# Optimization experiments

Measured on AMD Instinct MI355X. Metric: run time of the kernel, lower is better.

## Reference

```python
import jax, jax.numpy as jnp
import numpy as np

TEMPERATURE = 8.0  # sqrt(d_k)=sqrt(64)
NEG = -1000000000.0

def setup_inputs() -> dict:
    key = jax.random.key(0)
    kq, kk, kv, km = jax.random.split(key, 4)
    BH, S, D = 64, 1024, 64
    q = jax.random.normal(kq, (BH, S, D), dtype=jnp.float32)
    k = jax.random.normal(kk, (BH, S, D), dtype=jnp.float32)
    v = jax.random.normal(kv, (BH, S, D), dtype=jnp.float32)
    mask = jax.random.randint(km, (BH, 1, S), 0, 2).astype(jnp.int32)
    return {"q": q, "k": k, "v": v, "mask": mask}

def reference(q, k, v, mask):
    # attn scores: [BH, S, S]
    attn = jnp.einsum('bqd,bkd->bqk', q / TEMPERATURE, k)
    attn = jnp.where(mask == 0, NEG, attn)
    attn = jax.nn.softmax(attn, axis=-1)
    output = jnp.einsum('bqk,bkd->bqd', attn, v)
    return (output, attn)
```

## Files before the change

kernel.cpp:

```cpp
#include <hip/hip_runtime.h>
#include <hip/hip_bf16.h>
#include <stdint.h>

typedef unsigned short u16;
typedef u16 u16x8 __attribute__((ext_vector_type(8)));
typedef u16x8 __attribute__((may_alias)) u16x8a;
typedef float f32x4 __attribute__((ext_vector_type(4)));
typedef f32x4 __attribute__((may_alias)) f32x4a;
typedef __bf16 bf16x8 __attribute__((ext_vector_type(8)));
typedef float f32x16 __attribute__((ext_vector_type(16)));

#define S_LEN 1024
#define D_DIM 64
#define BHN   64

__device__ __forceinline__ u16 f2bf(float f) {
  unsigned u = __builtin_bit_cast(unsigned, f);
  return (u16)((u + 0x7fffu + ((u >> 16) & 1u)) >> 16);
}
__device__ __forceinline__ float bf2f(u16 b) {
  return __builtin_bit_cast(float, (unsigned)b << 16);
}
__device__ __forceinline__ bf16x8 cvt8(const float* p) {
  f32x4 a = *reinterpret_cast<const f32x4a*>(p);
  f32x4 b = *reinterpret_cast<const f32x4a*>(p + 4);
  u16x8 r;
#pragma unroll
  for (int j = 0; j < 4; ++j) { r[j] = f2bf(a[j]); r[4 + j] = f2bf(b[j]); }
  return __builtin_bit_cast(bf16x8, r);
}
__device__ __forceinline__ bf16x8 ldbf(const u16* p) {
  return __builtin_bit_cast(bf16x8, *reinterpret_cast<const u16x8a*>(p));
}

#define SMEM_BYTES 35456
#define RS_OFF     34816
#define INV_OFF    (34816 + 512)

__global__ __launch_bounds__(256, 3) void attn_kernel(
    const float* __restrict__ Q, const float* __restrict__ K, const int* __restrict__ Mk,
    const float* __restrict__ V, float* __restrict__ outO, float* __restrict__ outA) {
  __shared__ __align__(16) char smem[SMEM_BYTES];
  const int tid = threadIdx.x;
  const int wave = tid >> 6, lane = tid & 63;
  const int l31 = lane & 31, half = lane >> 5;

  const int id = blockIdx.x;
  const int bh = (id & 7) * 8 + ((id >> 3) & 7);
  const int q0 = (id >> 6) << 5;

  u16* tbase = (u16*)smem;
  float* rs_lds = (float*)(smem + RS_OFF);
  float* inv_lds = (float*)(smem + INV_OFF);

  const float* qb = Q + (((size_t)bh << 10) + q0 + l31) * D_DIM + half * 8;
  bf16x8 qa[4];
#pragma unroll
  for (int ks = 0; ks < 4; ++ks) qa[ks] = cvt8(qb + ks * 16);

  const int colbase = wave * 256;
  const float* kb0 = K + ((size_t)bh << 10) * D_DIM + half * 8;
  const int* mrow = Mk + ((size_t)bh << 10) + colbase + l31;

  bf16x8 pfrag[16];
  float rs[16];
#pragma unroll
  for (int r = 0; r < 16; ++r) rs[r] = 0.0f;

#pragma unroll
  for (int t = 0; t < 8; ++t) {
    u16* tile = tbase + (((t & 1) << 2) + wave) * (32 * 40);
    const int col0 = colbase + t * 32;
    const float* kb = kb0 + (size_t)(col0 + l31) * D_DIM;
    f32x16 acc = 0.0f;
#pragma unroll
    for (int ks = 0; ks < 4; ++ks) {
      bf16x8 kf = cvt8(kb + ks * 16);
      acc = __builtin_amdgcn_mfma_f32_32x32x16_bf16(qa[ks], kf, acc, 0, 0, 0);
    }
    const float mf = (mrow[t * 32] == 0) ? 0.0f : 1.0f;
#pragma unroll
    for (int r = 0; r < 16; ++r) {
      float p = exp2f(acc[r] * 0.18033688f) * mf;
      u16 pb16 = f2bf(p);
      rs[r] += bf2f(pb16);
      const int row = (r & 3) + ((r >> 2) << 3) + (half << 2);
      tile[row * 40 + l31] = pb16;
    }
    __syncthreads();
    pfrag[2 * t]     = ldbf(tile + l31 * 40 + half * 8);
    pfrag[2 * t + 1] = ldbf(tile + l31 * 40 + 16 + half * 8);
  }

#pragma unroll
  for (int r = 0; r < 16; ++r) {
    float s = rs[r];
#pragma unroll
    for (int m = 1; m < 32; m <<= 1) s += __shfl_xor(s, m, 64);
    rs[r] = s;
  }
  if (l31 == 0) {
#pragma unroll
    for (int r = 0; r < 16; ++r) {
      const int row = (r & 3) + ((r >> 2) << 3) + (half << 2);
      rs_lds[wave * 32 + row] = rs[r];
    }
  }
  __syncthreads();
  if (tid < 32) {
    float s = rs_lds[tid] + rs_lds[32 + tid] + rs_lds[64 + tid] + rs_lds[96 + tid];
    inv_lds[tid] = 1.0f / s;
  }
  __syncthreads();

  f32x16 oacc0 = 0.0f, oacc1 = 0.0f;
  const float* vb = V + (((size_t)bh << 10) + colbase + half * 8) * D_DIM + l31;
#pragma unroll
  for (int kk = 0; kk < 16; ++kk) {
    u16x8 b0u, b1u;
#pragma unroll
    for (int j = 0; j < 8; ++j) {
      b0u[j] = f2bf(vb[(kk * 16 + j) * D_DIM]);
      b1u[j] = f2bf(vb[(kk * 16 + j) * D_DIM + 32]);
    }
    bf16x8 b0 = __builtin_bit_cast(bf16x8, b0u);
    bf16x8 b1 = __builtin_bit_cast(bf16x8, b1u);
    oacc0 = __builtin_amdgcn_mfma_f32_32x32x16_bf16(pfrag[kk], b0, oacc0, 0, 0, 0);
    oacc1 = __builtin_amdgcn_mfma_f32_32x32x16_bf16(pfrag[kk], b1, oacc1, 0, 0, 0);
  }

  const float myinv = inv_lds[l31];
  float* ab = outA + ((size_t)bh << 20) + ((size_t)(q0 + l31) << 10) + colbase + half * 8;
#pragma unroll
  for (int t = 0; t < 8; ++t) {
#pragma unroll
    for (int f = 0; f < 2; ++f) {
      bf16x8 pf = pfrag[2 * t + f];
      f32x4 lo, hi;
#pragma unroll
      for (int j = 0; j < 4; ++j) {
        lo[j] = (float)pf[j] * myinv;
        hi[j] = (float)pf[4 + j] * myinv;
      }
      *reinterpret_cast<f32x4a*>(ab + t * 32 + f * 16) = lo;
      *reinterpret_cast<f32x4a*>(ab + t * 32 + f * 16 + 4) = hi;
    }
  }

  float* ored = (float*)smem;
#pragma unroll
  for (int r = 0; r < 16; ++r) {
    const int row = (r & 3) + ((r >> 2) << 3) + (half << 2);
    ored[(wave * 32 + row) * 68 + l31] = oacc0[r];
    ored[(wave * 32 + row) * 68 + 32 + l31] = oacc1[r];
  }
  __syncthreads();
  const int orow = tid >> 3;
  const int oc = (tid & 7) * 8;
  const float iv = inv_lds[orow];
  f32x4 o0, o1;
#pragma unroll
  for (int j = 0; j < 8; ++j) {
    float o = ored[orow * 68 + oc + j] + ored[(32 + orow) * 68 + oc + j] +
              ored[(64 + orow) * 68 + oc + j] + ored[(96 + orow) * 68 + oc + j];
    float v = o * iv;
    if (j < 4) o0[j] = v; else o1[j - 4] = v;
  }
  float* ob = outO + (((size_t)bh << 10) + q0 + orow) * D_DIM + oc;
  *reinterpret_cast<f32x4a*>(ob) = o0;
  *reinterpret_cast<f32x4a*>(ob + 4) = o1;
}

extern "C" void kernel_launch(void* const* d_in, const int* in_sizes, int n_in,
                              void* d_out, int out_size, void* d_ws, size_t ws_size,
                              hipStream_t stream) {
  (void)in_sizes; (void)n_in; (void)out_size; (void)d_ws; (void)ws_size;
  const float* Q = (const float*)d_in[0];
  const float* K = (const float*)d_in[1];
  const float* V = (const float*)d_in[2];
  const int*   M = (const int*)d_in[3];
  float* outO = (float*)d_out;
  float* outA = outO + (size_t)BHN * S_LEN * D_DIM;

  attn_kernel<<<dim3(BHN * (S_LEN / 32)), dim3(256), 0, stream>>>(Q, K, M, V, outO, outA);
}
```

Before: 428.6 us.

## Shrink LDS via atomic output reduction, drop per-tile barriers, interleave attn stores

Replaces the four-wave output reduction buffer with a single shared accumulator updated by LDS float atomics. This shrinks shared memory so four blocks per CU can be requested instead of three. The per-tile __syncthreads is replaced by a wave-local lgkmcnt wait, which is valid because each wave writes and reads only its own tile. The block-to-(bh, q0) mapping is changed so that consecutive blocks on the same XCD share K/V, and attention-probability stores are interleaved into the PV MFMA loop. Native __bf16 conversions replace the manual rounding helpers. The LDS atomics add serialization, and the accumulator must be zeroed up front.

```diff
diff --git a/kernel.cpp b/kernel.cpp
--- a/kernel.cpp
+++ b/kernel.cpp
@@ -1,5 +1,4 @@
 #include <hip/hip_runtime.h>
-#include <hip/hip_bf16.h>
 #include <stdint.h>
 
 typedef unsigned short u16;
@@ -14,30 +13,24 @@
 #define D_DIM 64
 #define BHN   64
 
-__device__ __forceinline__ u16 f2bf(float f) {
-  unsigned u = __builtin_bit_cast(unsigned, f);
-  return (u16)((u + 0x7fffu + ((u >> 16) & 1u)) >> 16);
-}
-__device__ __forceinline__ float bf2f(u16 b) {
-  return __builtin_bit_cast(float, (unsigned)b << 16);
-}
 __device__ __forceinline__ bf16x8 cvt8(const float* p) {
   f32x4 a = *reinterpret_cast<const f32x4a*>(p);
   f32x4 b = *reinterpret_cast<const f32x4a*>(p + 4);
-  u16x8 r;
+  bf16x8 r;
 #pragma unroll
-  for (int j = 0; j < 4; ++j) { r[j] = f2bf(a[j]); r[4 + j] = f2bf(b[j]); }
-  return __builtin_bit_cast(bf16x8, r);
+  for (int j = 0; j < 4; ++j) { r[j] = (__bf16)a[j]; r[4 + j] = (__bf16)b[j]; }
+  return r;
 }
 __device__ __forceinline__ bf16x8 ldbf(const u16* p) {
   return __builtin_bit_cast(bf16x8, *reinterpret_cast<const u16x8a*>(p));
 }
 
-#define SMEM_BYTES 35456
-#define RS_OFF     34816
-#define INV_OFF    (34816 + 512)
+#define ORED_OFF   20480
+#define RS_OFF     (ORED_OFF + 32 * 68 * 4)
+#define INV_OFF    (RS_OFF + 512)
+#define SMEM_BYTES (INV_OFF + 128)
 
-__global__ __launch_bounds__(256, 3) void attn_kernel(
+__global__ __launch_bounds__(256, 4) void attn_kernel(
     const float* __restrict__ Q, const float* __restrict__ K, const int* __restrict__ Mk,
     const float* __restrict__ V, float* __restrict__ outO, float* __restrict__ outA) {
   __shared__ __align__(16) char smem[SMEM_BYTES];
@@ -46,12 +39,16 @@
   const int l31 = lane & 31, half = lane >> 5;
 
   const int id = blockIdx.x;
-  const int bh = (id & 7) * 8 + ((id >> 3) & 7);
-  const int q0 = (id >> 6) << 5;
+  const int xcd = id & 7, ord = id >> 3;
+  const int bh = xcd * 8 + (ord >> 5);
+  const int q0 = (ord & 31) << 5;
 
   u16* tbase = (u16*)smem;
+  float* ored = (float*)(smem + ORED_OFF);
   float* rs_lds = (float*)(smem + RS_OFF);
   float* inv_lds = (float*)(smem + INV_OFF);
+
+  for (int i = tid; i < 32 * 68; i += 256) ored[i] = 0.0f;
 
   const float* qb = Q + (((size_t)bh << 10) + q0 + l31) * D_DIM + half * 8;
   bf16x8 qa[4];
@@ -70,8 +67,7 @@
 #pragma unroll
   for (int t = 0; t < 8; ++t) {
     u16* tile = tbase + (((t & 1) << 2) + wave) * (32 * 40);
-    const int col0 = colbase + t * 32;
-    const float* kb = kb0 + (size_t)(col0 + l31) * D_DIM;
+    const float* kb = kb0 + (size_t)(colbase + t * 32 + l31) * D_DIM;
     f32x16 acc = 0.0f;
 #pragma unroll
     for (int ks = 0; ks < 4; ++ks) {
@@ -82,12 +78,13 @@
 #pragma unroll
     for (int r = 0; r < 16; ++r) {
       float p = exp2f(acc[r] * 0.18033688f) * mf;
-      u16 pb16 = f2bf(p);
-      rs[r] += bf2f(pb16);
+      __bf16 pb = (__bf16)p;
+      rs[r] += (float)pb;
       const int row = (r & 3) + ((r >> 2) << 3) + (half << 2);
-      tile[row * 40 + l31] = pb16;
+      tile[row * 40 + l31] = __builtin_bit_cast(u16, pb);
     }
-    __syncthreads();
+    asm volatile("s_waitcnt lgkmcnt(0)" ::: "memory");
+    __builtin_amdgcn_sched_barrier(0);
     pfrag[2 * t]     = ldbf(tile + l31 * 40 + half * 8);
     pfrag[2 * t + 1] = ldbf(tile + l31 * 40 + 16 + half * 8);
   }
@@ -113,59 +110,48 @@
   }
   __syncthreads();
 
+  const float myinv = inv_lds[l31];
+  float* ab = outA + ((size_t)bh << 20) + ((size_t)(q0 + l31) << 10) + colbase + half * 8;
+  const float* vb = V + (((size_t)bh << 10) + colbase + half * 8) * D_DIM + l31;
   f32x16 oacc0 = 0.0f, oacc1 = 0.0f;
-  const float* vb = V + (((size_t)bh << 10) + colbase + half * 8) * D_DIM + l31;
 #pragma unroll
   for (int kk = 0; kk < 16; ++kk) {
-    u16x8 b0u, b1u;
+    bf16x8 b0, b1;
 #pragma unroll
-    for (int j = 0; j < 8; ++j) {
-      b0u[j] = f2bf(vb[(kk * 16 + j) * D_DIM]);
-      b1u[j] = f2bf(vb[(kk * 16 + j) * D_DIM + 32]);
+    for (int jj = 0; jj < 8; ++jj) {
+      b0[jj] = (__bf16)vb[(kk * 16 + jj) * D_DIM];
+      b1[jj] = (__bf16)vb[(kk * 16 + jj) * D_DIM + 32];
     }
-    bf16x8 b0 = __builtin_bit_cast(bf16x8, b0u);
-    bf16x8 b1 = __builtin_bit_cast(bf16x8, b1u);
     oacc0 = __builtin_amdgcn_mfma_f32_32x32x16_bf16(pfrag[kk], b0, oacc0, 0, 0, 0);
     oacc1 = __builtin_amdgcn_mfma_f32_32x32x16_bf16(pfrag[kk], b1, oacc1, 0, 0, 0);
+    f32x4 lo, hi;
+#pragma unroll
+    for (int jj = 0; jj < 4; ++jj) {
+      lo[jj] = (float)pfrag[kk][jj] * myinv;
+      hi[jj] = (float)pfrag[kk][4 + jj] * myinv;
+    }
+    float* dst = ab + (kk >> 1) * 32 + (kk & 1) * 16;
+    *reinterpret_cast<f32x4a*>(dst) = lo;
+    *reinterpret_cast<f32x4a*>(dst + 4) = hi;
   }
 
-  const float myinv = inv_lds[l31];
-  float* ab = outA + ((size_t)bh << 20) + ((size_t)(q0 + l31) << 10) + colbase + half * 8;
-#pragma unroll
-  for (int t = 0; t < 8; ++t) {
-#pragma unroll
-    for (int f = 0; f < 2; ++f) {
-      bf16x8 pf = pfrag[2 * t + f];
-      f32x4 lo, hi;
-#pragma unroll
-      for (int j = 0; j < 4; ++j) {
-        lo[j] = (float)pf[j] * myinv;
-        hi[j] = (float)pf[4 + j] * myinv;
-      }
-      *reinterpret_cast<f32x4a*>(ab + t * 32 + f * 16) = lo;
-      *reinterpret_cast<f32x4a*>(ab + t * 32 + f * 16 + 4) = hi;
-    }
-  }
-
-  float* ored = (float*)smem;
 #pragma unroll
   for (int r = 0; r < 16; ++r) {
     const int row = (r & 3) + ((r >> 2) << 3) + (half << 2);
-    ored[(wave * 32 + row) * 68 + l31] = oacc0[r];
-    ored[(wave * 32 + row) * 68 + 32 + l31] = oacc1[r];
+    atomicAdd(&ored[row * 68 + l31], oacc0[r]);
+    atomicAdd(&ored[row * 68 + 32 + l31], oacc1[r]);
   }
-  __syncthreads();
+  asm volatile("s_waitcnt lgkmcnt(0)" ::: "memory");
+  __builtin_amdgcn_s_barrier();
+  __builtin_amdgcn_sched_barrier(0);
+
   const int orow = tid >> 3;
   const int oc = (tid & 7) * 8;
   const float iv = inv_lds[orow];
-  f32x4 o0, o1;
+  f32x4 o0 = *reinterpret_cast<const f32x4a*>(ored + orow * 68 + oc);
+  f32x4 o1 = *reinterpret_cast<const f32x4a*>(ored + orow * 68 + oc + 4);
 #pragma unroll
-  for (int j = 0; j < 8; ++j) {
-    float o = ored[orow * 68 + oc + j] + ored[(32 + orow) * 68 + oc + j] +
-              ored[(64 + orow) * 68 + oc + j] + ored[(96 + orow) * 68 + oc + j];
-    float v = o * iv;
-    if (j < 4) o0[j] = v; else o1[j - 4] = v;
-  }
+  for (int jj = 0; jj < 4; ++jj) { o0[jj] *= iv; o1[jj] *= iv; }
   float* ob = outO + (((size_t)bh << 10) + q0 + orow) * D_DIM + oc;
   *reinterpret_cast<f32x4a*>(ob) = o0;
   *reinterpret_cast<f32x4a*>(ob + 4) = o1;
```

New measurement: 514.0 us. 1.2x slower.
